# Performance work log

Hardware: AMD Instinct MI355X
Metric: run time of the kernel (lower is better)

## Reference

```python
import jax, jax.numpy as jnp
import numpy as np
import math

B, S, DIM = 1, 2048, 4096
N_HEADS, N_KV, HEAD_DIM = 32, 8, 128
WINDOW = 2048
ROPE_THETA = 10000.0


def setup_inputs() -> dict:
    key = jax.random.key(0)
    ks = jax.random.split(key, 6)
    w_std = 0.02
    x = jax.random.normal(ks[0], (B, S, DIM), dtype=jnp.float32)
    wq = jax.random.normal(ks[1], (DIM, N_HEADS * HEAD_DIM), dtype=jnp.float32) * w_std
    wk = jax.random.normal(ks[2], (DIM, N_KV * HEAD_DIM), dtype=jnp.float32) * w_std
    wv = jax.random.normal(ks[3], (DIM, N_KV * HEAD_DIM), dtype=jnp.float32) * w_std
    wo = jax.random.normal(ks[4], (N_HEADS * HEAD_DIM, DIM), dtype=jnp.float32) * w_std
    # rotary tables (real/imag of complex_rotary_matrix)
    pos = jnp.arange(S, dtype=jnp.float32)
    inv_freq = 1.0 / (ROPE_THETA ** (jnp.arange(0, HEAD_DIM, 2, dtype=jnp.float32) / HEAD_DIM))
    angles = pos[:, None] * inv_freq[None, :]  # [S, HEAD_DIM/2]
    cos, sin = jnp.cos(angles), jnp.sin(angles)
    positions = jnp.arange(S, dtype=jnp.int32)
    # sliding-window causal additive mask: allow j <= i and i - j < WINDOW
    i = jnp.arange(S)[:, None]
    j = jnp.arange(S)[None, :]
    allowed = (j <= i) & (i - j < WINDOW)
    mask = jnp.where(allowed, 0.0, -jnp.inf).astype(jnp.float32)
    cache_k = jnp.zeros((B, WINDOW, N_KV, HEAD_DIM), dtype=jnp.float32)
    cache_v = jnp.zeros((B, WINDOW, N_KV, HEAD_DIM), dtype=jnp.float32)
    return dict(x=x, wq=wq, wk=wk, wv=wv, wo=wo, cos=cos, sin=sin,
                positions=positions, mask=mask, cache_k=cache_k, cache_v=cache_v)


def _apply_rope(t, cos, sin):
    # t: [B, S, H, D]; interleaved complex pairs as in torch.view_as_complex
    tp = t.reshape(*t.shape[:-1], HEAD_DIM // 2, 2)
    te, to = tp[..., 0], tp[..., 1]
    c = cos[None, :, None, :]
    s = sin[None, :, None, :]
    re = te * c - to * s
    im = te * s + to * c
    return jnp.stack([re, im], axis=-1).reshape(t.shape)


def reference(x, wq, wk, wv, wo, cos, sin, positions, mask, cache_k, cache_v):
    repeats = N_HEADS // N_KV
    q = (x @ wq).reshape(B, S, N_HEADS, HEAD_DIM)
    k = (x @ wk).reshape(B, S, N_KV, HEAD_DIM)
    v = (x @ wv).reshape(B, S, N_KV, HEAD_DIM)
    q = _apply_rope(q, cos, sin)
    k = _apply_rope(k, cos, sin)
    # rolling KV-cache scatter update (prefill path: positions.shape[0] > 1)
    scatter_pos = positions[-WINDOW:] % WINDOW
    new_cache_k = cache_k.at[:, scatter_pos].set(k[:, -WINDOW:])
    new_cache_v = cache_v.at[:, scatter_pos].set(v[:, -WINDOW:])
    # GQA head repetition (repeat_kv_head)
    k = jnp.repeat(k, repeats, axis=2)  # [B, S, N_HEADS, D]
    v = jnp.repeat(v, repeats, axis=2)
    scores = jnp.einsum('bqhd,bkhd->bhqk', q, k) / math.sqrt(HEAD_DIM)
    scores = scores + mask[None, None, :, :]
    attn = jax.nn.softmax(scores.astype(jnp.float32), axis=-1).astype(q.dtype)
    out = jnp.einsum('bhqk,bkhd->bqhd', attn, v)
    out = out.reshape(B, S, N_HEADS * HEAD_DIM)
    return out @ wo, new_cache_k, new_cache_v
```

## Files before the change

### kernel.cpp

```cpp
#include <hip/hip_runtime.h>

typedef __bf16 bf16;
typedef __bf16 bf16x8 __attribute__((ext_vector_type(8)));
typedef __bf16 bf16x4 __attribute__((ext_vector_type(4)));
typedef float  f32x4  __attribute__((ext_vector_type(4)));

__device__ __forceinline__ f32x4 mfma16(bf16x8 a, bf16x8 b, f32x4 c) {
  return __builtin_amdgcn_mfma_f32_16x16x32_bf16(a, b, c, 0, 0, 0);
}

__device__ __forceinline__ void gload16(const bf16* g, bf16* l) {
  __builtin_amdgcn_global_load_lds(
      (const __attribute__((address_space(1))) void*)g,
      (__attribute__((address_space(3))) void*)l, 16, 0, 0);
}

__global__ void cast_x_kernel(const float* __restrict__ in, bf16* __restrict__ out) {
  const int i = blockIdx.x * 256 + threadIdx.x;
  const float4 v = ((const float4*)in)[i];
  bf16x4 o;
  o[0] = (bf16)v.x; o[1] = (bf16)v.y; o[2] = (bf16)v.z; o[3] = (bf16)v.w;
  *(bf16x4*)&out[(size_t)i * 4] = o;
}

__global__ void transpose_cast(const float* __restrict__ in, bf16* __restrict__ out,
                               int ldin, int ldout) {
  __shared__ bf16 t[32][33];
  const int c0 = blockIdx.x * 32, r0 = blockIdx.y * 32;
  const int x = threadIdx.x, y = threadIdx.y;
  #pragma unroll
  for (int i = 0; i < 32; i += 8)
    t[y + i][x] = (bf16)in[(size_t)(r0 + y + i) * ldin + c0 + x];
  __syncthreads();
  #pragma unroll
  for (int i = 0; i < 32; i += 8)
    out[(size_t)(c0 + y + i) * ldout + r0 + x] = t[x][y + i];
}

__global__ void permute_v(const bf16* __restrict__ qkv, bf16* __restrict__ vp) {
  __shared__ bf16 t[32][33];
  const int sb  = blockIdx.x;
  const int kvh = blockIdx.y >> 2;
  const int dt  = blockIdx.y & 3;
  const int x = threadIdx.x, y = threadIdx.y;
  #pragma unroll
  for (int i = 0; i < 32; i += 8)
    t[y + i][x] = qkv[(size_t)(sb * 32 + y + i) * 6144 + 5120 + kvh * 128 + dt * 32 + x];
  __syncthreads();
  #pragma unroll
  for (int i = 0; i < 32; i += 8)
    vp[((size_t)(kvh * 64 + sb) * 128 + dt * 32 + y + i) * 32 + x] = t[x][y + i];
}

#define MMQ(MB, NB)                                                            \
  _Pragma("unroll")                                                            \
  for (int mi = 0; mi < 4; ++mi)                                               \
    _Pragma("unroll")                                                          \
    for (int ni = 0; ni < 2; ++ni)                                             \
      _Pragma("unroll")                                                        \
      for (int kk = 0; kk < 2; ++kk)                                           \
        acc[MB + mi][NB + ni] =                                                \
            mfma16(ar[mi][kk], br[NB + ni][kk], acc[MB + mi][NB + ni]);

#define PH_OPEN                                                                \
  __builtin_amdgcn_s_barrier();                                                \
  asm volatile("s_waitcnt lgkmcnt(0)" ::: "memory");                           \
  __builtin_amdgcn_s_setprio(1);

#define PH_CLOSE                                                               \
  __builtin_amdgcn_s_setprio(0);                                               \
  __builtin_amdgcn_s_barrier();

template <typename OutT, int NSPLIT>
__global__ __launch_bounds__(512, 2)
void gemm8(const bf16* __restrict__ A, const bf16* __restrict__ Bt,
           OutT* __restrict__ C0, OutT* __restrict__ C1,
           int M, int N, int K, int ldc) {
  __shared__ __attribute__((aligned(16))) bf16 lds[65536];
  char* ldsc = (char*)lds;
  constexpr int AO0 = 0, BO0 = 32768, AO1 = 65536, BO1 = 98304;

  const int t    = threadIdx.x;
  const int w    = t >> 6;
  const int lane = t & 63;
  const int l15  = lane & 15;
  const int lg   = lane >> 4;
  const int wm   = w >> 2;
  const int wn   = w & 3;
  const int hb   = wn >> 1;

  const int nbm = M >> 8;
  const int nb2 = nbm * NSPLIT;
  const int cpx = (nb2 * (N >> 8)) >> 3;
  const int lid = ((int)blockIdx.x & 7) * cpx + ((int)blockIdx.x >> 3);
  const int bn  = (lid / nb2) * 256;
  const int rem = lid % nb2;
  const int kh  = rem / nbm;
  const int bm  = (rem % nbm) * 256;
  const int Kloc = K / NSPLIT;
  const int koff = kh * Kloc;
  OutT* __restrict__ C = (NSPLIT == 2 && kh) ? C1 : C0;

  const int d0     = t * 16;
  const int dsw    = d0 ^ (((d0 >> 9) & 1) << 5);
  const int srow_s = (dsw >> 6) & 127;
  const int scol_e = (dsw & 63) >> 1;

  auto stg = [&](const bf16* P, int rowbase, int tile, int half, int region) {
    const bf16* s = P + (size_t)(rowbase + half * 128 + srow_s) * K +
                    koff + tile * 64 + scol_e;
    gload16(s,      (bf16*)(ldsc + region + half * 16384 + w * 1024));
    gload16(s + 32, (bf16*)(ldsc + region + half * 16384 + 8192 + w * 1024));
  };
  auto lda = [&](int AO, int m, int kk) -> bf16x8 {
    int byte = AO + wm * 16384 + kk * 8192 + (m * 16 + l15) * 64 + lg * 16;
    byte ^= ((byte >> 9) & 1) << 5;
    return *(const bf16x8*)(ldsc + byte);
  };
  auto ldb = [&](int BO, int n, int kk) -> bf16x8 {
    int byte = BO + hb * 16384 + kk * 8192 +
               ((wn & 1) * 64 + n * 16 + l15) * 64 + lg * 16;
    byte ^= ((byte >> 9) & 1) << 5;
    return *(const bf16x8*)(ldsc + byte);
  };

  f32x4 acc[8][4] = {};
  bf16x8 ar[4][2], br[4][2];

  const int NT = Kloc >> 6;
  const int NI = Kloc >> 7;

  stg(A,  bm, 0, 0, AO0);  stg(A,  bm, 0, 1, AO0);
  stg(Bt, bn, 0, 0, BO0);  stg(Bt, bn, 0, 1, BO0);
  stg(Bt, bn, 1, 0, BO1);  stg(Bt, bn, 1, 1, BO1);
  asm volatile("s_waitcnt vmcnt(4)" ::: "memory");
  __builtin_amdgcn_s_barrier();

  #pragma unroll 1
  for (int it = 0; it < NI; ++it) {
    const int t1 = 2 * it + 1;
    const int t2 = (2 * it + 2 < NT) ? 2 * it + 2 : NT - 1;
    const int t3 = (2 * it + 3 < NT) ? 2 * it + 3 : NT - 1;

    #pragma unroll
    for (int mi = 0; mi < 4; ++mi) {
      ar[mi][0] = lda(AO0, mi, 0); ar[mi][1] = lda(AO0, mi, 1);
    }
    #pragma unroll
    for (int ni = 0; ni < 2; ++ni) {
      br[ni][0] = ldb(BO0, ni, 0); br[ni][1] = ldb(BO0, ni, 1);
    }
    stg(A, bm, t1, 0, AO1);
    PH_OPEN; MMQ(0, 0); PH_CLOSE;
    #pragma unroll
    for (int ni = 2; ni < 4; ++ni) {
      br[ni][0] = ldb(BO0, ni, 0); br[ni][1] = ldb(BO0, ni, 1);
    }
    stg(A, bm, t1, 1, AO1);
    PH_OPEN; MMQ(0, 2); PH_CLOSE;
    #pragma unroll
    for (int mi = 0; mi < 4; ++mi) {
      ar[mi][0] = lda(AO0, 4 + mi, 0); ar[mi][1] = lda(AO0, 4 + mi, 1);
    }
    stg(Bt, bn, t2, 0, BO0);
    PH_OPEN; MMQ(4, 0); PH_CLOSE;
    stg(Bt, bn, t2, 1, BO0);
    PH_OPEN; MMQ(4, 2);
    __builtin_amdgcn_s_setprio(0);
    asm volatile("s_waitcnt vmcnt(4)" ::: "memory");
    __builtin_amdgcn_s_barrier();
    #pragma unroll
    for (int mi = 0; mi < 4; ++mi) {
      ar[mi][0] = lda(AO1, mi, 0); ar[mi][1] = lda(AO1, mi, 1);
    }
    #pragma unroll
    for (int ni = 0; ni < 2; ++ni) {
      br[ni][0] = ldb(BO1, ni, 0); br[ni][1] = ldb(BO1, ni, 1);
    }
    stg(A, bm, t2, 0, AO0);
    PH_OPEN; MMQ(0, 0); PH_CLOSE;
    #pragma unroll
    for (int ni = 2; ni < 4; ++ni) {
      br[ni][0] = ldb(BO1, ni, 0); br[ni][1] = ldb(BO1, ni, 1);
    }
    stg(A, bm, t2, 1, AO0);
    PH_OPEN; MMQ(0, 2); PH_CLOSE;
    #pragma unroll
    for (int mi = 0; mi < 4; ++mi) {
      ar[mi][0] = lda(AO1, 4 + mi, 0); ar[mi][1] = lda(AO1, 4 + mi, 1);
    }
    stg(Bt, bn, t3, 0, BO1);
    PH_OPEN; MMQ(4, 0); PH_CLOSE;
    stg(Bt, bn, t3, 1, BO1);
    PH_OPEN; MMQ(4, 2);
    __builtin_amdgcn_s_setprio(0);
    asm volatile("s_waitcnt vmcnt(4)" ::: "memory");
    __builtin_amdgcn_s_barrier();
  }

  #pragma unroll
  for (int mi = 0; mi < 8; ++mi)
    #pragma unroll
    for (int ni = 0; ni < 4; ++ni)
      #pragma unroll
      for (int rr = 0; rr < 4; ++rr)
        C[(size_t)(bm + wm * 128 + mi * 16 + lg * 4 + rr) * ldc +
          (bn + wn * 64 + ni * 16 + l15)] = (OutT)acc[mi][ni][rr];
}

__global__ void reduce_out(const bf16* __restrict__ p0, const bf16* __restrict__ p1,
                           float* __restrict__ out) {
  const int i = blockIdx.x * 256 + threadIdx.x;
  const bf16x4 a = *(const bf16x4*)&p0[(size_t)i * 4];
  const bf16x4 b = *(const bf16x4*)&p1[(size_t)i * 4];
  float4 o;
  o.x = (float)a[0] + (float)b[0];
  o.y = (float)a[1] + (float)b[1];
  o.z = (float)a[2] + (float)b[2];
  o.w = (float)a[3] + (float)b[3];
  *(float4*)&out[(size_t)i * 4] = o;
}

__global__ void rope_q_kernel(bf16* __restrict__ q, const float* __restrict__ cs,
                              const float* __restrict__ sn) {
  const int idx = blockIdx.x * 256 + threadIdx.x;
  const int p  = idx & 63;
  const int sh = idx >> 6;
  const int h  = sh & 31;
  const int s  = sh >> 5;
  const float c  = cs[s * 64 + p];
  const float si = sn[s * 64 + p];
  const size_t ii = (size_t)s * 6144 + h * 128 + 2 * p;
  const float te = (float)q[ii], to = (float)q[ii + 1];
  q[ii]     = (bf16)(te * c - to * si);
  q[ii + 1] = (bf16)(te * si + to * c);
}

__global__ void rope_k_kernel(const bf16* __restrict__ qkv, bf16* __restrict__ kp,
                              float* __restrict__ ck, const float* __restrict__ cs,
                              const float* __restrict__ sn) {
  const int idx = blockIdx.x * 256 + threadIdx.x;
  const int p  = idx & 63;
  const int sh = idx >> 6;
  const int h  = sh & 7;
  const int s  = sh >> 3;
  const float c  = cs[s * 64 + p];
  const float si = sn[s * 64 + p];
  const size_t ii = (size_t)s * 6144 + 4096 + h * 128 + 2 * p;
  const float te = (float)qkv[ii], to = (float)qkv[ii + 1];
  const float re = te * c - to * si;
  const float im = te * si + to * c;
  const size_t io = ((size_t)(h * 4 + (p >> 4)) * 2048 + s) * 32 + ((2 * p) & 31);
  kp[io]     = (bf16)re;
  kp[io + 1] = (bf16)im;
  const size_t ic = (size_t)s * 1024 + h * 128 + 2 * p;
  ck[ic]     = re;
  ck[ic + 1] = im;
}

__global__ void cast_v_kernel(const bf16* __restrict__ qkv, float* __restrict__ cv) {
  const int i = blockIdx.x * 256 + threadIdx.x;
  const int s = i >> 8;
  const int c = (i & 255) * 4;
  const bf16x4 v = *(const bf16x4*)&qkv[(size_t)s * 6144 + 5120 + c];
  float4 o;
  o.x = (float)v[0]; o.y = (float)v[1]; o.z = (float)v[2]; o.w = (float)v[3];
  *(float4*)&cv[(size_t)s * 1024 + c] = o;
}

__global__ __launch_bounds__(256, 3)
void attn_fwd(const bf16* __restrict__ Q, const bf16* __restrict__ Kp,
              const bf16* __restrict__ Vp, bf16* __restrict__ O) {
  __shared__ __attribute__((aligned(16))) bf16 Kb[8192];
  __shared__ __attribute__((aligned(16))) bf16 Vb[8192];
  __shared__ __attribute__((aligned(16))) bf16 P_lds[4][16][72];
  const int id   = blockIdx.x;
  const int qt   = 31 - (id >> 5);
  const int kvh  = id & 7;
  const int sub  = (id >> 3) & 3;
  const int h    = kvh * 4 + sub;
  const int t    = threadIdx.x;
  const int w    = t >> 6;
  const int lane = t & 63;
  const int l15  = lane & 15;
  const int lg   = lane >> 4;
  const float scale = 0.08838834764831845f;
  const bf16* Kh = Kp + (size_t)kvh * 262144;
  const bf16* Vh = Vp + (size_t)kvh * 262144;
  const int koff = (t >> 2) * 32 + (t & 3) * 8;

  const int qw  = qt * 64 + w * 16;
  const int myq = qw + l15;

  bf16x8 qf[4];
  #pragma unroll
  for (int ds = 0; ds < 4; ++ds)
    qf[ds] = *(const bf16x8*)&Q[(size_t)myq * 6144 + h * 128 + ds * 32 + lg * 8];

  f32x4 o[8] = {};
  float m = -1e30f, ell = 0.f;

  #pragma unroll
  for (int i = 0; i < 4; ++i)
    gload16(Kh + (size_t)i * 65536 + koff, Kb + i * 2048 + w * 512);
  #pragma unroll
  for (int i = 0; i < 4; ++i)
    gload16(Vh + (size_t)i * 2048 + koff, Vb + i * 2048 + w * 512);
  __syncthreads();

  #pragma unroll 1
  for (int kt = 0; kt <= qt; ++kt) {
    f32x4 T[4] = {};
    __builtin_amdgcn_s_setprio(1);
    #pragma unroll
    for (int kb = 0; kb < 4; ++kb)
      #pragma unroll
      for (int ds = 0; ds < 4; ++ds) {
        bf16x8 kf = *(const bf16x8*)&Kb[(ds * 64 + kb * 16 + l15) * 32 + lg * 8];
        T[kb] = mfma16(kf, qf[ds], T[kb]);
      }
    __builtin_amdgcn_s_setprio(0);
    __syncthreads();
    if (kt < qt) {
      #pragma unroll
      for (int i = 0; i < 4; ++i)
        gload16(Kh + (size_t)i * 65536 + (kt + 1) * 2048 + koff,
                Kb + i * 2048 + w * 512);
    }

    float pv[16];
    float pmax = -1e30f;
    if (kt == qt) {
      #pragma unroll
      for (int kb = 0; kb < 4; ++kb)
        #pragma unroll
        for (int r = 0; r < 4; ++r) {
          const int key = qt * 64 + kb * 16 + lg * 4 + r;
          const float s = (key > myq) ? -1e30f : T[kb][r] * scale;
          pv[kb * 4 + r] = s;
          pmax = fmaxf(pmax, s);
        }
    } else {
      #pragma unroll
      for (int kb = 0; kb < 4; ++kb)
        #pragma unroll
        for (int r = 0; r < 4; ++r) {
          const float s = T[kb][r] * scale;
          pv[kb * 4 + r] = s;
          pmax = fmaxf(pmax, s);
        }
    }
    float base = m;
    if (!__all(pmax - m <= 8.f)) {
      float wmax = pmax;
      wmax = fmaxf(wmax, __shfl_xor(wmax, 16));
      wmax = fmaxf(wmax, __shfl_xor(wmax, 32));
      const float newm = fmaxf(m, wmax);
      const float corr = __expf(m - newm);
      ell *= corr;
      m = newm; base = newm;
      float sf[4];
      #pragma unroll
      for (int r = 0; r < 4; ++r) sf[r] = __shfl(corr, lg * 4 + r);
      #pragma unroll
      for (int df = 0; df < 8; ++df)
        #pragma unroll
        for (int r = 0; r < 4; ++r) o[df][r] *= sf[r];
    }
    bf16 pb[16];
    float tsum = 0.f;
    #pragma unroll
    for (int i = 0; i < 16; ++i) {
      const float p = __expf(pv[i] - base);
      tsum += p;
      pb[i] = (bf16)p;
    }
    ell += tsum;

    #pragma unroll
    for (int kb = 0; kb < 4; ++kb) {
      bf16x4 pk;
      pk[0] = pb[kb * 4 + 0]; pk[1] = pb[kb * 4 + 1];
      pk[2] = pb[kb * 4 + 2]; pk[3] = pb[kb * 4 + 3];
      *(bf16x4*)&P_lds[w][l15][kb * 16 + lg * 4] = pk;
    }
    __builtin_amdgcn_s_setprio(1);
    #pragma unroll
    for (int ks = 0; ks < 2; ++ks) {
      bf16x8 pa = *(const bf16x8*)&P_lds[w][l15][ks * 32 + lg * 8];
      #pragma unroll
      for (int df = 0; df < 8; ++df) {
        bf16x8 vf = *(const bf16x8*)&Vb[(ks * 128 + df * 16 + l15) * 32 + lg * 8];
        o[df] = mfma16(pa, vf, o[df]);
      }
    }
    __builtin_amdgcn_s_setprio(0);
    __syncthreads();
    if (kt < qt) {
      #pragma unroll
      for (int i = 0; i < 4; ++i)
        gload16(Vh + (size_t)(kt + 1) * 8192 + i * 2048 + koff,
                Vb + i * 2048 + w * 512);
    }
  }

  ell += __shfl_xor(ell, 16);
  ell += __shfl_xor(ell, 32);
  float er[4];
  #pragma unroll
  for (int r = 0; r < 4; ++r) er[r] = 1.f / __shfl(ell, lg * 4 + r);
  #pragma unroll
  for (int df = 0; df < 8; ++df)
    #pragma unroll
    for (int r = 0; r < 4; ++r)
      O[(size_t)(qw + lg * 4 + r) * 4096 + h * 128 + df * 16 + l15] =
          (bf16)(o[df][r] * er[r]);
}

extern "C" void kernel_launch(void* const* d_in, const int* in_sizes, int n_in,
                              void* d_out, int out_size, void* d_ws, size_t ws_size,
                              hipStream_t stream) {
  const float* x    = (const float*)d_in[0];
  const float* wq   = (const float*)d_in[1];
  const float* wk   = (const float*)d_in[2];
  const float* wv   = (const float*)d_in[3];
  const float* wo   = (const float*)d_in[4];
  const float* cosf_ = (const float*)d_in[5];
  const float* sinf_ = (const float*)d_in[6];

  float* out     = (float*)d_out;
  float* cache_k = out + (size_t)8388608;
  float* cache_v = cache_k + (size_t)2097152;
  bf16* qkv = (bf16*)d_out;

  bf16* ws = (bf16*)d_ws;
  bf16* wT = ws;
  bf16* kp = ws + (size_t)25165824;
  bf16* vp = kp + (size_t)2097152;
  bf16* xb = vp + (size_t)2097152;
  bf16* aout = xb;
  bf16* part1 = wT + (size_t)16777216;
  bf16* part0 = ws + (size_t)37748736;

  const dim3 tb(32, 8);
  cast_x_kernel<<<8192, 256, 0, stream>>>(x, xb);
  transpose_cast<<<dim3(128, 128), tb, 0, stream>>>(wq, wT, 4096, 4096);
  transpose_cast<<<dim3(32, 128), tb, 0, stream>>>(wk, wT + (size_t)16777216,
                                                   1024, 4096);
  transpose_cast<<<dim3(32, 128), tb, 0, stream>>>(wv, wT + (size_t)20971520,
                                                   1024, 4096);
  gemm8<bf16, 1><<<192, 512, 0, stream>>>(xb, wT, qkv, qkv, 2048, 6144, 4096, 6144);
  rope_q_kernel<<<16384, 256, 0, stream>>>(qkv, cosf_, sinf_);
  rope_k_kernel<<<4096, 256, 0, stream>>>(qkv, kp, cache_k, cosf_, sinf_);
  cast_v_kernel<<<2048, 256, 0, stream>>>(qkv, cache_v);
  permute_v<<<dim3(64, 32), tb, 0, stream>>>(qkv, vp);
  transpose_cast<<<dim3(128, 128), tb, 0, stream>>>(wo, wT, 4096, 4096);
  attn_fwd<<<1024, 256, 0, stream>>>(qkv, kp, vp, aout);
  gemm8<bf16, 2><<<256, 512, 0, stream>>>(aout, wT, part0, part1,
                                          2048, 4096, 4096, 4096);
  reduce_out<<<8192, 256, 0, stream>>>(part0, part1, out);
}
```

Before: 329.3 us.

## Double-buffer K/V tiles in attention and fuse V cache cast into permute

The attention kernel now keeps two LDS buffers each for K and V and issues the next tile's loads at the start of the iteration. This lets the loads overlap the QK, softmax and PV compute and drops one barrier per iteration. LDS use roughly doubles, so launch bounds drop from 3 to 2 blocks per CU, which lowers occupancy. Separately, the fp32 cache_v write moves into permute_v, removing the cast_v_kernel launch, though those stores are now scalar rather than vectorized.

```diff
diff --git a/kernel.cpp b/kernel.cpp
--- a/kernel.cpp
+++ b/kernel.cpp
@@ -37,15 +37,19 @@
     out[(size_t)(c0 + y + i) * ldout + r0 + x] = t[x][y + i];
 }
 
-__global__ void permute_v(const bf16* __restrict__ qkv, bf16* __restrict__ vp) {
+__global__ void permute_v(const bf16* __restrict__ qkv, bf16* __restrict__ vp,
+                          float* __restrict__ cv) {
   __shared__ bf16 t[32][33];
   const int sb  = blockIdx.x;
   const int kvh = blockIdx.y >> 2;
   const int dt  = blockIdx.y & 3;
   const int x = threadIdx.x, y = threadIdx.y;
   #pragma unroll
-  for (int i = 0; i < 32; i += 8)
-    t[y + i][x] = qkv[(size_t)(sb * 32 + y + i) * 6144 + 5120 + kvh * 128 + dt * 32 + x];
+  for (int i = 0; i < 32; i += 8) {
+    const bf16 v = qkv[(size_t)(sb * 32 + y + i) * 6144 + 5120 + kvh * 128 + dt * 32 + x];
+    t[y + i][x] = v;
+    cv[(size_t)(sb * 32 + y + i) * 1024 + kvh * 128 + dt * 32 + x] = (float)v;
+  }
   __syncthreads();
   #pragma unroll
   for (int i = 0; i < 32; i += 8)
@@ -258,21 +262,11 @@
   ck[ic + 1] = im;
 }
 
-__global__ void cast_v_kernel(const bf16* __restrict__ qkv, float* __restrict__ cv) {
-  const int i = blockIdx.x * 256 + threadIdx.x;
-  const int s = i >> 8;
-  const int c = (i & 255) * 4;
-  const bf16x4 v = *(const bf16x4*)&qkv[(size_t)s * 6144 + 5120 + c];
-  float4 o;
-  o.x = (float)v[0]; o.y = (float)v[1]; o.z = (float)v[2]; o.w = (float)v[3];
-  *(float4*)&cv[(size_t)s * 1024 + c] = o;
-}
-
-__global__ __launch_bounds__(256, 3)
+__global__ __launch_bounds__(256, 2)
 void attn_fwd(const bf16* __restrict__ Q, const bf16* __restrict__ Kp,
               const bf16* __restrict__ Vp, bf16* __restrict__ O) {
-  __shared__ __attribute__((aligned(16))) bf16 Kb[8192];
-  __shared__ __attribute__((aligned(16))) bf16 Vb[8192];
+  __shared__ __attribute__((aligned(16))) bf16 Kb[2][8192];
+  __shared__ __attribute__((aligned(16))) bf16 Vb[2][8192];
   __shared__ __attribute__((aligned(16))) bf16 P_lds[4][16][72];
   const int id   = blockIdx.x;
   const int qt   = 31 - (id >> 5);
@@ -302,31 +296,36 @@
 
   #pragma unroll
   for (int i = 0; i < 4; ++i)
-    gload16(Kh + (size_t)i * 65536 + koff, Kb + i * 2048 + w * 512);
+    gload16(Kh + (size_t)i * 65536 + koff, &Kb[0][i * 2048 + w * 512]);
   #pragma unroll
   for (int i = 0; i < 4; ++i)
-    gload16(Vh + (size_t)i * 2048 + koff, Vb + i * 2048 + w * 512);
+    gload16(Vh + (size_t)i * 2048 + koff, &Vb[0][i * 2048 + w * 512]);
   __syncthreads();
 
+  int cur = 0;
   #pragma unroll 1
   for (int kt = 0; kt <= qt; ++kt) {
+    if (kt < qt) {
+      #pragma unroll
+      for (int i = 0; i < 4; ++i)
+        gload16(Kh + (size_t)i * 65536 + (kt + 1) * 2048 + koff,
+                &Kb[cur ^ 1][i * 2048 + w * 512]);
+      #pragma unroll
+      for (int i = 0; i < 4; ++i)
+        gload16(Vh + (size_t)(kt + 1) * 8192 + i * 2048 + koff,
+                &Vb[cur ^ 1][i * 2048 + w * 512]);
+    }
+
     f32x4 T[4] = {};
     __builtin_amdgcn_s_setprio(1);
     #pragma unroll
     for (int kb = 0; kb < 4; ++kb)
       #pragma unroll
       for (int ds = 0; ds < 4; ++ds) {
-        bf16x8 kf = *(const bf16x8*)&Kb[(ds * 64 + kb * 16 + l15) * 32 + lg * 8];
+        bf16x8 kf = *(const bf16x8*)&Kb[cur][(ds * 64 + kb * 16 + l15) * 32 + lg * 8];
         T[kb] = mfma16(kf, qf[ds], T[kb]);
       }
     __builtin_amdgcn_s_setprio(0);
-    __syncthreads();
-    if (kt < qt) {
-      #pragma unroll
-      for (int i = 0; i < 4; ++i)
-        gload16(Kh + (size_t)i * 65536 + (kt + 1) * 2048 + koff,
-                Kb + i * 2048 + w * 512);
-    }
 
     float pv[16];
     float pmax = -1e30f;
@@ -390,18 +389,13 @@
       bf16x8 pa = *(const bf16x8*)&P_lds[w][l15][ks * 32 + lg * 8];
       #pragma unroll
       for (int df = 0; df < 8; ++df) {
-        bf16x8 vf = *(const bf16x8*)&Vb[(ks * 128 + df * 16 + l15) * 32 + lg * 8];
+        bf16x8 vf = *(const bf16x8*)&Vb[cur][(ks * 128 + df * 16 + l15) * 32 + lg * 8];
         o[df] = mfma16(pa, vf, o[df]);
       }
     }
     __builtin_amdgcn_s_setprio(0);
     __syncthreads();
-    if (kt < qt) {
-      #pragma unroll
-      for (int i = 0; i < 4; ++i)
-        gload16(Vh + (size_t)(kt + 1) * 8192 + i * 2048 + koff,
-                Vb + i * 2048 + w * 512);
-    }
+    cur ^= 1;
   }
 
   ell += __shfl_xor(ell, 16);
@@ -452,8 +446,7 @@
   gemm8<bf16, 1><<<192, 512, 0, stream>>>(xb, wT, qkv, qkv, 2048, 6144, 4096, 6144);
   rope_q_kernel<<<16384, 256, 0, stream>>>(qkv, cosf_, sinf_);
   rope_k_kernel<<<4096, 256, 0, stream>>>(qkv, kp, cache_k, cosf_, sinf_);
-  cast_v_kernel<<<2048, 256, 0, stream>>>(qkv, cache_v);
-  permute_v<<<dim3(64, 32), tb, 0, stream>>>(qkv, vp);
+  permute_v<<<dim3(64, 32), tb, 0, stream>>>(qkv, vp, cache_v);
   transpose_cast<<<dim3(128, 128), tb, 0, stream>>>(wo, wT, 4096, 4096);
   attn_fwd<<<1024, 256, 0, stream>>>(qkv, kp, vp, aout);
   gemm8<bf16, 2><<<256, 512, 0, stream>>>(aout, wT, part0, part1,
```

After: 336.3 us. 1.02x slower.
